# Optimization experiments

Hardware: AMD Instinct MI355X
Metric: run time of the kernel (lower is better)

Reference implementation:

```python
import jax, jax.numpy as jnp
import numpy as np

WIN = 10  # self.len in the torch module


def setup_inputs() -> dict:
    key = jax.random.key(0)
    # [batch, seq_length, agent_num, vel]
    inputs = jax.random.normal(key, (8, 512, 96, 2), dtype=jnp.float32)
    return {"inputs": inputs}


def reference(inputs):
    # Faithful vectorization of the triple loop:
    #                    / sqrt(sum xc_i^2 * sum xc_j^2)
    # (the (seq_length*vel - 1) normalizers in cov/std cancel exactly)
    B, S, A, V = inputs.shape
    xc = inputs - inputs.mean(axis=1, keepdims=True)  # center over time
    # per-timestep pairwise Gram over the tiny vel dim: [B, S, A, A]
    g = jnp.einsum('bsiv,bsjv->bsij', xc, xc)
    # sliding-window sums via cumulative-sum trick
    C = jnp.cumsum(g, axis=1)                         # [B, S, A, A]
    head = C[:, :S - 1]                               # window end at step s (s=1..S-1)
    tail = jnp.concatenate(
        [jnp.zeros((B, WIN, A, A), C.dtype), C[:, :S - 1 - WIN]], axis=1)
    W = head - tail                                   # windowed Gram [B, S-1, A, A]
    d = jnp.diagonal(W, axis1=2, axis2=3)             # windowed energy [B, S-1, A]
    corr = W / jnp.sqrt(d[..., :, None] * d[..., None, :])
    # torch code never writes the diagonal -> stays zero
    mask = 1.0 - jnp.eye(A, dtype=corr.dtype)
    return corr * mask
```

## Files before the change

### kernel.cpp

```cpp
#include <hip/hip_runtime.h>

constexpr int WIN = 10;
constexpr int Bn  = 8;
constexpr int Sn  = 512;
constexpr int An  = 96;
constexpr int Vn  = 2;
constexpr int Tn  = Sn - 1;
constexpr int AV  = An * Vn;

constexpr int SCHUNK = 32;
constexpr int NCH    = Sn / SCHUNK;
constexpr int CH     = 8;
constexpr int CHUNKS_PER_B = (Tn + CH - 1) / CH;
constexpr int MAXROWS = CH + WIN - 1;

__global__ __launch_bounds__(192)
void partial_kernel(const float* __restrict__ in, float* __restrict__ partial) {
    const int blk = blockIdx.x;
    const int b   = blk / NCH;
    const int c   = blk - b * NCH;
    const int av  = threadIdx.x;
    const float* p = in + ((size_t)(b * Sn + c * SCHUNK)) * AV + av;
    float acc = 0.f;
    #pragma unroll
    for (int s = 0; s < SCHUNK; ++s) acc += p[(size_t)s * AV];
    partial[(size_t)blk * AV + av] = acc;
}

__global__ __launch_bounds__(256)
void reduce_kernel(const float* __restrict__ partial, float* __restrict__ sums) {
    int idx = blockIdx.x * blockDim.x + threadIdx.x;
    if (idx >= Bn * AV) return;
    int b  = idx / AV;
    int av = idx - b * AV;
    float acc = 0.f;
    #pragma unroll
    for (int c = 0; c < NCH; ++c) acc += partial[(size_t)(b * NCH + c) * AV + av];
    sums[idx] = acc;
}

__global__ __launch_bounds__(256)
void corr_kernel(const float* __restrict__ in, const float* __restrict__ sums,
                 float* __restrict__ out) {
    __shared__ float xw[MAXROWS * AV];

    const int bid   = blockIdx.x;
    const int b     = bid / CHUNKS_PER_B;
    const int chunk = bid - b * CHUNKS_PER_B;
    const int t0    = chunk * CH;
    const int t1    = min(t0 + CH - 1, Tn - 1);
    int sbase = t0 - (WIN - 1); if (sbase < 0) sbase = 0;
    const int nrows = t1 - sbase + 1;

    const int tid = threadIdx.x;

    {
        const float2* src = reinterpret_cast<const float2*>(
            in + ((size_t)(b * Sn + sbase)) * AV);
        const float2* mb = reinterpret_cast<const float2*>(sums + b * AV);
        float2* dst = reinterpret_cast<float2*>(xw);
        const int tot2 = nrows * (AV / 2);
        constexpr float invS = 1.0f / Sn;
        for (int idx = tid; idx < tot2; idx += 256) {
            int av2 = idx % (AV / 2);
            float2 v = src[idx], m = mb[av2];
            dst[idx] = make_float2(v.x - m.x * invS, v.y - m.y * invS);
        }
    }
    __syncthreads();

    const int tx = tid & 31;
    const int ty = tid >> 5;

    float acc[12][3];
    float di[12], dj[3];
    #pragma unroll
    for (int r = 0; r < 12; ++r) {
        di[r] = 0.f;
        #pragma unroll
        for (int c = 0; c < 3; ++c) acc[r][c] = 0.f;
    }
    #pragma unroll
    for (int c = 0; c < 3; ++c) dj[c] = 0.f;

    auto accum = [&](int ls, float sgn) {
        const float* xs = &xw[ls * AV];
        float2 xj[3];
        #pragma unroll
        for (int c = 0; c < 3; ++c) {
            xj[c] = *reinterpret_cast<const float2*>(&xs[(tx + 32 * c) * 2]);
            dj[c] += sgn * (xj[c].x * xj[c].x + xj[c].y * xj[c].y);
        }
        #pragma unroll
        for (int r = 0; r < 12; ++r) {
            float2 x = *reinterpret_cast<const float2*>(&xs[(ty + 8 * r) * 2]);
            float2 xs2 = make_float2(sgn * x.x, sgn * x.y);
            di[r] += xs2.x * x.x + xs2.y * x.y;
            #pragma unroll
            for (int c = 0; c < 3; ++c)
                acc[r][c] += xs2.x * xj[c].x + xs2.y * xj[c].y;
        }
    };

    auto emit = [&](int t) {
        float rsj[3];
        #pragma unroll
        for (int c = 0; c < 3; ++c) rsj[c] = rsqrtf(dj[c]);
        float* ob = out + (size_t)(b * Tn + t) * (An * An);
        #pragma unroll
        for (int r = 0; r < 12; ++r) {
            int i = ty + 8 * r;
            float ri = rsqrtf(di[r]);
            #pragma unroll
            for (int c = 0; c < 3; ++c) {
                int j = tx + 32 * c;
                float v = (i == j) ? 0.f : acc[r][c] * ri * rsj[c];
                ob[(size_t)i * An + j] = v;
            }
        }
    };

    for (int s = sbase; s <= t0; ++s) accum(s - sbase, 1.0f);
    emit(t0);

    for (int t = t0 + 1; t <= t1; ++t) {
        accum(t - sbase, 1.0f);
        if (t >= WIN) accum(t - WIN - sbase, -1.0f);
        emit(t);
    }
}

extern "C" void kernel_launch(void* const* d_in, const int* in_sizes, int n_in,
                              void* d_out, int out_size, void* d_ws, size_t ws_size,
                              hipStream_t stream) {
    const float* in = (const float*)d_in[0];
    float* out = (float*)d_out;
    float* sums    = (float*)d_ws;
    float* partial = (float*)d_ws + Bn * AV;

    partial_kernel<<<Bn * NCH, 192, 0, stream>>>(in, partial);
    reduce_kernel<<<(Bn * AV + 255) / 256, 256, 0, stream>>>(partial, sums);
    corr_kernel<<<Bn * CHUNKS_PER_B, 256, 0, stream>>>(in, sums, out);
}
```

Before: 42.25 us.

## Split output rows across two blocks, vectorize staging loads, drop sign multiply

```diff
diff --git a/kernel.cpp b/kernel.cpp
--- a/kernel.cpp
+++ b/kernel.cpp
@@ -4,15 +4,16 @@
 constexpr int Bn  = 8;
 constexpr int Sn  = 512;
 constexpr int An  = 96;
-constexpr int Vn  = 2;
 constexpr int Tn  = Sn - 1;
-constexpr int AV  = An * Vn;
+constexpr int AV  = An * 2;
 
 constexpr int SCHUNK = 32;
 constexpr int NCH    = Sn / SCHUNK;
 constexpr int CH     = 8;
 constexpr int CHUNKS_PER_B = (Tn + CH - 1) / CH;
 constexpr int MAXROWS = CH + WIN - 1;
+constexpr int ISPLIT  = 2;
+constexpr int RPT     = (An / ISPLIT) / 8;
 
 __global__ __launch_bounds__(192)
 void partial_kernel(const float* __restrict__ in, float* __restrict__ partial) {
@@ -45,26 +46,32 @@
     __shared__ float xw[MAXROWS * AV];
 
     const int bid   = blockIdx.x;
-    const int b     = bid / CHUNKS_PER_B;
-    const int chunk = bid - b * CHUNKS_PER_B;
-    const int t0    = chunk * CH;
-    const int t1    = min(t0 + CH - 1, Tn - 1);
+    const int b     = bid / (CHUNKS_PER_B * ISPLIT);
+    const int rem   = bid - b * (CHUNKS_PER_B * ISPLIT);
+    const int chunk = rem >> 1;
+    const int half  = rem & 1;
+    const int i0    = half * (An / ISPLIT);
+
+    const int t0 = chunk * CH;
+    const int t1 = min(t0 + CH - 1, Tn - 1);
     int sbase = t0 - (WIN - 1); if (sbase < 0) sbase = 0;
     const int nrows = t1 - sbase + 1;
 
     const int tid = threadIdx.x;
 
     {
-        const float2* src = reinterpret_cast<const float2*>(
+        const float4* src = reinterpret_cast<const float4*>(
             in + ((size_t)(b * Sn + sbase)) * AV);
-        const float2* mb = reinterpret_cast<const float2*>(sums + b * AV);
-        float2* dst = reinterpret_cast<float2*>(xw);
-        const int tot2 = nrows * (AV / 2);
+        const float4* mb = reinterpret_cast<const float4*>(sums + b * AV);
+        float4* dst = reinterpret_cast<float4*>(xw);
+        const int tot4 = nrows * (AV / 4);
         constexpr float invS = 1.0f / Sn;
-        for (int idx = tid; idx < tot2; idx += 256) {
-            int av2 = idx % (AV / 2);
-            float2 v = src[idx], m = mb[av2];
-            dst[idx] = make_float2(v.x - m.x * invS, v.y - m.y * invS);
+        for (int idx = tid; idx < tot4; idx += 256) {
+            int av4 = idx % (AV / 4);
+            float4 v = src[idx], m = mb[av4];
+            v.x -= m.x * invS; v.y -= m.y * invS;
+            v.z -= m.z * invS; v.w -= m.w * invS;
+            dst[idx] = v;
         }
     }
     __syncthreads();
@@ -72,10 +79,10 @@
     const int tx = tid & 31;
     const int ty = tid >> 5;
 
-    float acc[12][3];
-    float di[12], dj[3];
+    float acc[RPT][3];
+    float di[RPT], dj[3];
     #pragma unroll
-    for (int r = 0; r < 12; ++r) {
+    for (int r = 0; r < RPT; ++r) {
         di[r] = 0.f;
         #pragma unroll
         for (int c = 0; c < 3; ++c) acc[r][c] = 0.f;
@@ -83,24 +90,25 @@
     #pragma unroll
     for (int c = 0; c < 3; ++c) dj[c] = 0.f;
 
-    auto accum = [&](int ls, float sgn) {
-        const float* xs = &xw[ls * AV];
-        float2 xj[3];
-        #pragma unroll
-        for (int c = 0; c < 3; ++c) {
-            xj[c] = *reinterpret_cast<const float2*>(&xs[(tx + 32 * c) * 2]);
-            dj[c] += sgn * (xj[c].x * xj[c].x + xj[c].y * xj[c].y);
-        }
-        #pragma unroll
-        for (int r = 0; r < 12; ++r) {
-            float2 x = *reinterpret_cast<const float2*>(&xs[(ty + 8 * r) * 2]);
-            float2 xs2 = make_float2(sgn * x.x, sgn * x.y);
-            di[r] += xs2.x * x.x + xs2.y * x.y;
-            #pragma unroll
-            for (int c = 0; c < 3; ++c)
-                acc[r][c] += xs2.x * xj[c].x + xs2.y * xj[c].y;
-        }
-    };
+#define ACCUM(ls, OP)                                                       \
+    {                                                                       \
+        const float* xs = &xw[(ls) * AV];                                   \
+        float2 xj[3];                                                       \
+        _Pragma("unroll")                                                   \
+        for (int c = 0; c < 3; ++c) {                                       \
+            xj[c] = *reinterpret_cast<const float2*>(&xs[(tx + 32 * c) * 2]);\
+            dj[c] OP (xj[c].x * xj[c].x + xj[c].y * xj[c].y);               \
+        }                                                                   \
+        _Pragma("unroll")                                                   \
+        for (int r = 0; r < RPT; ++r) {                                     \
+            float2 xi = *reinterpret_cast<const float2*>(                   \
+                &xs[(i0 + ty + 8 * r) * 2]);                                \
+            di[r] OP (xi.x * xi.x + xi.y * xi.y);                           \
+            _Pragma("unroll")                                               \
+            for (int c = 0; c < 3; ++c)                                     \
+                acc[r][c] OP (xi.x * xj[c].x + xi.y * xj[c].y);             \
+        }                                                                   \
+    }
 
     auto emit = [&](int t) {
         float rsj[3];
@@ -108,8 +116,8 @@
         for (int c = 0; c < 3; ++c) rsj[c] = rsqrtf(dj[c]);
         float* ob = out + (size_t)(b * Tn + t) * (An * An);
         #pragma unroll
-        for (int r = 0; r < 12; ++r) {
-            int i = ty + 8 * r;
+        for (int r = 0; r < RPT; ++r) {
+            int i = i0 + ty + 8 * r;
             float ri = rsqrtf(di[r]);
             #pragma unroll
             for (int c = 0; c < 3; ++c) {
@@ -120,14 +128,15 @@
         }
     };
 
-    for (int s = sbase; s <= t0; ++s) accum(s - sbase, 1.0f);
+    for (int s = sbase; s <= t0; ++s) ACCUM(s - sbase, +=);
     emit(t0);
 
     for (int t = t0 + 1; t <= t1; ++t) {
-        accum(t - sbase, 1.0f);
-        if (t >= WIN) accum(t - WIN - sbase, -1.0f);
+        ACCUM(t - sbase, +=);
+        if (t >= WIN) ACCUM(t - WIN - sbase, -=);
         emit(t);
     }
+#undef ACCUM
 }
 
 extern "C" void kernel_launch(void* const* d_in, const int* in_sizes, int n_in,
@@ -140,5 +149,5 @@
 
     partial_kernel<<<Bn * NCH, 192, 0, stream>>>(in, partial);
     reduce_kernel<<<(Bn * AV + 255) / 256, 256, 0, stream>>>(partial, sums);
-    corr_kernel<<<Bn * CHUNKS_PER_B, 256, 0, stream>>>(in, sums, out);
+    corr_kernel<<<Bn * CHUNKS_PER_B * ISPLIT, 256, 0, stream>>>(in, sums, out);
 }
```

Result: faster. 40.92 us (-3.1%).
